# Kernel tuning notes

Hardware: AMD Instinct MI355X
Metric: run time of the kernel (lower is better)

The kernel has to match this reference:

```python
import jax, jax.numpy as jnp
import numpy as np

B, T, D = 4, 4096, 2048
E, C = 8, 512
O = 2048
I = D // E  # expert_in_features = 256


def setup_inputs() -> dict:
    key = jax.random.key(0)
    k1, k2, k3, k4, k5 = jax.random.split(key, 5)
    x = jax.random.normal(k1, (B, T, D), dtype=jnp.float32)
    combine_array = jax.random.uniform(k2, (B, T, E, C), dtype=jnp.float32)
    dispatch_mask = jax.random.uniform(k3, (B, T, E, C), dtype=jnp.float32)
    weight = jax.random.normal(k4, (E, O, I), dtype=jnp.float32) * (1.0 / np.sqrt(I))
    bias = jax.random.normal(k5, (O,), dtype=jnp.float32) * 0.01
    return {"x": x, "combine_array": combine_array, "dispatch_mask": dispatch_mask,
            "weight": weight, "bias": bias}


def reference(x, combine_array, dispatch_mask, weight, bias):
    b, t, d = x.shape
    e, o, i = weight.shape
    # dispatch: one-hot gather of tokens into expert capacity slots
    xr = x.reshape(b, t, e, i)                                   # [B,T,E,I]
    xd = jnp.einsum('btei,btec->beci', xr, dispatch_mask)        # [B,E,C,I]
    # bias homogenization trick: append 1 to features, bias column to weight
    x_homo = jnp.concatenate([xd, jnp.ones_like(xd[..., :1])], axis=-1)       # [B,E,C,I+1]
    b_col = jnp.broadcast_to(bias.reshape(1, o, 1), (e, o, 1))
    w_homo = jnp.concatenate([weight, b_col], axis=-1)                        # [E,O,I+1]
    # per-expert linear then combine scatter back to tokens
    y = jnp.einsum('beci,eoi->beco', x_homo, w_homo)             # [B,E,C,O]
    out = jnp.einsum('beco,btec->bto', y, combine_array)         # [B,T,O]
    return out
```

## Files before the change

kernel.cpp:

```cpp
#include <hip/hip_runtime.h>

typedef float f32x4 __attribute__((ext_vector_type(4)));
typedef short s16x8 __attribute__((ext_vector_type(8)));
typedef short s16x4 __attribute__((ext_vector_type(4)));
typedef unsigned u32x4 __attribute__((ext_vector_type(4)));
typedef unsigned u32x2 __attribute__((ext_vector_type(2)));

#define DEVI __device__ __forceinline__

static constexpr int B_ = 4, T_ = 4096, D_ = 2048, E_ = 8, C_ = 512, O_ = 2048, I_ = 256;
static constexpr size_t XDN = (size_t)B_ * E_ * I_ * C_;

DEVI short f2bf(float f) {
  unsigned u = __builtin_bit_cast(unsigned, f);
  u += 0x7FFFu + ((u >> 16) & 1u);
  return (short)(u >> 16);
}

DEVI unsigned cvtpk(float lo, float hi) {
  unsigned r;
  asm("v_cvt_pk_bf16_f32 %0, %1, %2" : "=v"(r) : "v"(lo), "v"(hi));
  return r;
}

DEVI void gll16(const short* gsrc, short* ldst) {
  __builtin_amdgcn_global_load_lds(
      (const __attribute__((address_space(1))) void*)gsrc,
      (__attribute__((address_space(3))) void*)ldst, 16, 0, 0);
}

__global__ __launch_bounds__(512, 2) void k_gemm1(const float* __restrict__ x,
                                                  const float* __restrict__ disp,
                                                  const float* __restrict__ w,
                                                  short* __restrict__ wT,
                                                  float* __restrict__ xdP) {
  __shared__ short lXT[128 * 64];
  __shared__ short lDT[256 * 64];
  const int tid = threadIdx.x;
  const int bid = blockIdx.x;

  if (bid >= 256) {
    const int pb = bid - 256;
#pragma unroll
    for (int u = 0; u < 2; u++) {
      const int idx = (pb * 512 + tid) * 2 + u;
      const int o = idx >> 9;
      const int dd = (idx & 511) << 2;
      const int e = dd >> 8, i = dd & 255;
      f32x4 v = *(const f32x4*)(w + (((size_t)e * O_ + o) * I_ + i));
      u32x2 p = {cvtpk(v[0], v[1]), cvtpk(v[2], v[3])};
      const int dsw = (dd & ~63) | (dd & 7) | ((((dd >> 3) & 7) ^ (o & 7)) << 3);
      *(u32x2*)(wT + (size_t)o * D_ + dsw) = p;
    }
    return;
  }

  const int xcd = bid & 7, slot = bid >> 3;
  const int grp = (slot >> 2) * 8 + xcd;
  const int jj = slot & 3;
  const int be = grp >> 1, kc = grp & 1;
  const int mt = jj >> 1, nt = jj & 1;
  const int b = be >> 3, e = be & 7;
  const int lane = tid & 63, wid = tid >> 6;
  const int wm = wid >> 2, wn = wid & 3;
  const int g = lane >> 4, lr = lane & 15;

  const size_t xbase = (size_t)b * T_ * D_ + (size_t)e * I_ + (size_t)mt * 128;
  const size_t dbase = (size_t)b * T_ * (E_ * C_) + (size_t)e * C_ + (size_t)nt * 256;

  const f32x4 z4 = {0.f, 0.f, 0.f, 0.f};
  f32x4 acc[4][4];
#pragma unroll
  for (int i = 0; i < 4; i++)
#pragma unroll
    for (int j = 0; j < 4; j++) acc[i][j] = z4;

  const int xt0 = (tid >> 4) * 2;
  const int xi8 = (tid & 15) * 8;
  const int dt0 = (tid >> 5) * 2;
  const int dc8 = (tid & 31) * 8;
  const int q7 = tid & 7;

  f32x4 xa0, xa1, xb0, xb1;
  f32x4 da[2][4];
  auto loadRegs = [&](int kt) {
    const float* sx = x + xbase + (size_t)(kt + xt0) * D_ + xi8;
    xa0 = *(const f32x4*)sx;
    xa1 = *(const f32x4*)(sx + 4);
    xb0 = *(const f32x4*)(sx + D_);
    xb1 = *(const f32x4*)(sx + D_ + 4);
#pragma unroll
    for (int tt = 0; tt < 2; tt++) {
      const float* sd = disp + dbase + (size_t)(kt + tt * 32 + dt0) * (E_ * C_) + dc8;
      da[tt][0] = *(const f32x4*)sd;
      da[tt][1] = *(const f32x4*)(sd + 4);
      da[tt][2] = *(const f32x4*)(sd + E_ * C_);
      da[tt][3] = *(const f32x4*)(sd + E_ * C_ + 4);
    }
  };
  auto writeLds = [&]() {
#pragma unroll
    for (int j = 0; j < 8; j++) {
      const int i = xi8 + j;
      const int ad = i * 64 + (xt0 ^ ((j ^ q7) << 3));
      float va = (j < 4) ? xa0[j] : xa1[j - 4];
      float vb = (j < 4) ? xb0[j] : xb1[j - 4];
      *(unsigned*)&lXT[ad] = cvtpk(va, vb);
    }
#pragma unroll
    for (int tt = 0; tt < 2; tt++)
#pragma unroll
      for (int j = 0; j < 8; j++) {
        const int c = dc8 + j;
        const int ad = c * 64 + ((tt * 32 + dt0) ^ ((j ^ q7) << 3));
        float ua = (j < 4) ? da[tt][0][j] : da[tt][1][j - 4];
        float ub = (j < 4) ? da[tt][2][j] : da[tt][3][j - 4];
        *(unsigned*)&lDT[ad] = cvtpk(ua, ub);
      }
  };

  const int k0 = kc * 2048, kend = k0 + 2048;
  loadRegs(k0);
  for (int kt = k0; kt < kend; kt += 64) {
    __syncthreads();
    writeLds();
    if (kt + 64 < kend) loadRegs(kt + 64);
    __syncthreads();
#pragma unroll
    for (int kk = 0; kk < 2; kk++) {
      const int tb = kk * 32 + g * 8;
      s16x8 af[4], bfr[4];
#pragma unroll
      for (int mi = 0; mi < 4; mi++) {
        const int r = wm * 64 + mi * 16 + lr;
        const int sws = (((r & 7) ^ ((r >> 3) & 7)) << 3);
        af[mi] = *(const s16x8*)&lXT[r * 64 + (tb ^ sws)];
      }
#pragma unroll
      for (int ni = 0; ni < 4; ni++) {
        const int r = wn * 64 + ni * 16 + lr;
        const int sws = (((r & 7) ^ ((r >> 3) & 7)) << 3);
        bfr[ni] = *(const s16x8*)&lDT[r * 64 + (tb ^ sws)];
      }
#pragma unroll
      for (int mi = 0; mi < 4; mi++)
#pragma unroll
        for (int ni = 0; ni < 4; ni++)
          acc[mi][ni] = __builtin_amdgcn_mfma_f32_16x16x32_bf16(af[mi], bfr[ni], acc[mi][ni], 0, 0, 0);
    }
  }

  float* op = xdP + (size_t)kc * XDN + (size_t)be * I_ * C_;
#pragma unroll
  for (int mi = 0; mi < 4; mi++)
#pragma unroll
    for (int ni = 0; ni < 4; ni++)
#pragma unroll
      for (int r = 0; r < 4; r++) {
        const int ig = mt * 128 + wm * 64 + mi * 16 + g * 4 + r;
        const int cg = nt * 256 + wn * 64 + ni * 16 + lr;
        op[(size_t)ig * C_ + cg] = acc[mi][ni][r];
      }
}

__global__ __launch_bounds__(256) void k_cvt(const float* __restrict__ xdP,
                                             short* __restrict__ xdT) {
  size_t idx = (size_t)blockIdx.x * 256 + threadIdx.x;
  f32x4 a = *(const f32x4*)(xdP + idx * 4);
  f32x4 b = *(const f32x4*)(xdP + XDN + idx * 4);
#pragma unroll
  for (int j = 0; j < 4; j++) a[j] += b[j];
  u32x2 p = {cvtpk(a[0], a[1]), cvtpk(a[2], a[3])};
  *(u32x2*)(xdT + idx * 4) = p;
}

__global__ __launch_bounds__(512, 2) void k_zgemm(const float* __restrict__ comb,
                                                  const short* __restrict__ xdT,
                                                  short* __restrict__ z,
                                                  float* __restrict__ Se) {
  __shared__ short lA[128 * 64];
  __shared__ short lB[256 * 64];
  const int tid = threadIdx.x;
  const int bid = blockIdx.x;
  const int be = bid >> 5, mt = bid & 31;
  const int b = be >> 3, e = be & 7;
  const int lane = tid & 63, wid = tid >> 6;
  const int wm = wid >> 2, wn = wid & 3;
  const int g = lane >> 4, lr = lane & 15;

  const size_t abase = (size_t)b * T_ * (E_ * C_) + (size_t)(mt * 128) * (E_ * C_) + (size_t)e * C_;
  const short* Bsrc = xdT + (size_t)be * I_ * C_;

  float rs[2] = {0.f, 0.f};
  const f32x4 z4 = {0.f, 0.f, 0.f, 0.f};
  f32x4 acc[4][4];
#pragma unroll
  for (int i = 0; i < 4; i++)
#pragma unroll
    for (int j = 0; j < 4; j++) acc[i][j] = z4;

  for (int ct = 0; ct < C_; ct += 64) {
    __syncthreads();
#pragma unroll
    for (int cc = 0; cc < 2; cc++) {
      const int q = tid + 512 * cc;
      const int row = q >> 3;
      const int k8 = (q & 7) << 3;
      const int sw = (row & 7) << 3;
      const float* sa = comb + abase + (size_t)row * (E_ * C_) + ct + k8;
      f32x4 a0 = *(const f32x4*)sa;
      f32x4 a1 = *(const f32x4*)(sa + 4);
      rs[cc] += a0[0] + a0[1] + a0[2] + a0[3] + a1[0] + a1[1] + a1[2] + a1[3];
      u32x4 pw = {cvtpk(a0[0], a0[1]), cvtpk(a0[2], a0[3]),
                  cvtpk(a1[0], a1[1]), cvtpk(a1[2], a1[3])};
      *(u32x4*)&lA[row * 64 + (k8 ^ sw)] = pw;
    }
#pragma unroll
    for (int cc = 0; cc < 4; cc++) {
      const int q = tid + 512 * cc;
      const int row = q >> 3;
      const int k8 = (q & 7) << 3;
      const int sw = (row & 7) << 3;
      s16x8 pb = *(const s16x8*)(Bsrc + (size_t)row * C_ + ct + k8);
      *(s16x8*)&lB[row * 64 + (k8 ^ sw)] = pb;
    }
    __syncthreads();
#pragma unroll
    for (int kk = 0; kk < 2; kk++) {
      const int kb = kk * 32 + g * 8;
      s16x8 af[4], bf[4];
#pragma unroll
      for (int mi = 0; mi < 4; mi++) {
        const int r = wm * 64 + mi * 16 + lr;
        af[mi] = *(const s16x8*)&lA[r * 64 + (kb ^ ((r & 7) << 3))];
      }
#pragma unroll
      for (int ni = 0; ni < 4; ni++) {
        const int r = wn * 64 + ni * 16 + lr;
        bf[ni] = *(const s16x8*)&lB[r * 64 + (kb ^ ((r & 7) << 3))];
      }
#pragma unroll
      for (int mi = 0; mi < 4; mi++)
#pragma unroll
        for (int ni = 0; ni < 4; ni++)
          acc[mi][ni] = __builtin_amdgcn_mfma_f32_16x16x32_bf16(af[mi], bf[ni], acc[mi][ni], 0, 0, 0);
    }
  }
#pragma unroll
  for (int cc = 0; cc < 2; cc++) {
    float v = rs[cc];
    v += __shfl_xor(v, 1);
    v += __shfl_xor(v, 2);
    v += __shfl_xor(v, 4);
    if ((tid & 7) == 0)
      Se[((size_t)b * E_ + e) * T_ + mt * 128 + (tid >> 3) + 64 * cc] = v;
  }
#pragma unroll
  for (int mi = 0; mi < 4; mi++)
#pragma unroll
    for (int ni = 0; ni < 4; ni++)
#pragma unroll
      for (int r = 0; r < 4; r++) {
        const int tg = mt * 128 + wm * 64 + mi * 16 + g * 4 + r;
        const int ig = wn * 64 + ni * 16 + lr;
        const int d = e * I_ + ig;
        const int dsw = (d & ~63) | (d & 7) | ((((d >> 3) & 7) ^ (tg & 7)) << 3);
        z[((size_t)b * T_ + tg) * D_ + dsw] = f2bf(acc[mi][ni][r]);
      }
}

__global__ __launch_bounds__(512, 2) void k_outgemm(const short* __restrict__ z,
                                                    const short* __restrict__ wT,
                                                    const float* __restrict__ bias,
                                                    const float* __restrict__ Se,
                                                    float* __restrict__ out) {
  __shared__ short lA[256 * 64];
  __shared__ short lB[256 * 64];
  const int tid = threadIdx.x;
  const int lane = tid & 63, wid = tid >> 6;
  const int wm = wid >> 2, wn = wid & 3;
  const int g = lane >> 4, lr = lane & 15;

  const int bid = blockIdx.x;
  const int swz = (bid & 7) * 64 + (bid >> 3);
  const int mt = swz >> 3, nt = swz & 7;
  const int row0 = mt * 256;
  const int col0 = nt * 256;

  const int srow = (wid << 4) + (lane >> 3);
  const int scol = (lane & 7) << 3;
  const short* Abase = z + (size_t)(row0 + srow) * D_ + scol;
  const short* Bbase = wT + (size_t)(col0 + srow) * D_ + scol;

  const f32x4 zero4 = {0.f, 0.f, 0.f, 0.f};
  f32x4 acc[8][4];
#pragma unroll
  for (int i = 0; i < 8; i++)
#pragma unroll
    for (int j = 0; j < 4; j++) acc[i][j] = zero4;

  s16x8 af[8], bf0[4], bf1[4];
  const int swr = (lr & 7) << 3;

  auto stage = [&](int dt) {
#pragma unroll
    for (int h = 0; h < 2; h++) {
      gll16(Abase + (size_t)(h * 128) * D_ + dt, &lA[(h * 128 + wid * 16) * 64]);
      gll16(Abase + (size_t)(h * 128 + 8) * D_ + dt, &lA[(h * 128 + wid * 16 + 8) * 64]);
      gll16(Bbase + (size_t)(h * 128) * D_ + dt, &lB[(h * 128 + wid * 16) * 64]);
      gll16(Bbase + (size_t)(h * 128 + 8) * D_ + dt, &lB[(h * 128 + wid * 16 + 8) * 64]);
    }
  };
  auto readA = [&](int mh) {
#pragma unroll
    for (int mi = 0; mi < 4; mi++) {
      const int r = mh * 128 + wm * 64 + mi * 16 + lr;
#pragma unroll
      for (int ks = 0; ks < 2; ks++)
        af[mi * 2 + ks] = *(const s16x8*)&lA[r * 64 + ((ks * 32 + g * 8) ^ swr)];
    }
  };
  auto readB = [&](int nh, s16x8* arr) {
#pragma unroll
    for (int ni = 0; ni < 2; ni++) {
      const int r = nh * 128 + wn * 32 + ni * 16 + lr;
#pragma unroll
      for (int ks = 0; ks < 2; ks++)
        arr[ni * 2 + ks] = *(const s16x8*)&lB[r * 64 + ((ks * 32 + g * 8) ^ swr)];
    }
  };
  auto mmaq = [&](int mh, int nh, const s16x8* bb) {
    __builtin_amdgcn_s_setprio(1);
#pragma unroll
    for (int mi = 0; mi < 4; mi++)
#pragma unroll
      for (int ni = 0; ni < 2; ni++)
#pragma unroll
        for (int ks = 0; ks < 2; ks++)
          acc[mh * 4 + mi][nh * 2 + ni] = __builtin_amdgcn_mfma_f32_16x16x32_bf16(
              af[mi * 2 + ks], bb[ni * 2 + ks], acc[mh * 4 + mi][nh * 2 + ni], 0, 0, 0);
    __builtin_amdgcn_s_setprio(0);
  };

  for (int t = 0; t < 32; ++t) {
    __syncthreads();
    stage(t * 64);
    __syncthreads();
    readA(0); readB(0, bf0);
    mmaq(0, 0, bf0);
    readB(1, bf1);
    mmaq(0, 1, bf1);
    readA(1);
    mmaq(1, 0, bf0);
    mmaq(1, 1, bf1);
  }

  __syncthreads();
  float* sS = (float*)lA;
  if (tid < 256) {
    const int bb = row0 >> 12, tt = (row0 & (T_ - 1)) + tid;
    float s = 0.f;
#pragma unroll
    for (int e = 0; e < E_; e++)
      s += Se[((size_t)(bb * E_ + e) << 12) + tt];
    sS[tid] = s;
  }
  __syncthreads();

  float bia[4];
#pragma unroll
  for (int nh = 0; nh < 2; nh++)
#pragma unroll
    for (int ni = 0; ni < 2; ni++)
      bia[nh * 2 + ni] = bias[col0 + nh * 128 + wn * 32 + ni * 16 + lr];
#pragma unroll
  for (int mh = 0; mh < 2; mh++)
#pragma unroll
    for (int mi = 0; mi < 4; mi++)
#pragma unroll
      for (int r = 0; r < 4; r++) {
        const int tg = row0 + mh * 128 + wm * 64 + mi * 16 + g * 4 + r;
        const float s = sS[tg - row0];
#pragma unroll
        for (int nh = 0; nh < 2; nh++)
#pragma unroll
          for (int ni = 0; ni < 2; ni++) {
            const int og = col0 + nh * 128 + wn * 32 + ni * 16 + lr;
            out[(size_t)tg * O_ + og] = acc[mh * 4 + mi][nh * 2 + ni][r] + bia[nh * 2 + ni] * s;
          }
      }
}

extern "C" void kernel_launch(void* const* d_in, const int* in_sizes, int n_in,
                              void* d_out, int out_size, void* d_ws, size_t ws_size,
                              hipStream_t stream) {
  const float* x    = (const float*)d_in[0];
  const float* comb = (const float*)d_in[1];
  const float* disp = (const float*)d_in[2];
  const float* w    = (const float*)d_in[3];
  const float* bias = (const float*)d_in[4];
  float* out = (float*)d_out;

  char* ws = (char*)d_ws;
  short* wT  = (short*)(ws);
  short* xdT = (short*)(ws + 8388608);
  short* z   = (short*)(ws + 16777216);
  float* xdP = (float*)(ws + 16777216);
  float* Se  = (float*)(ws + 83886080);

  k_gemm1<<<dim3(1280), dim3(512), 0, stream>>>(x, disp, w, wT, xdP);
  k_cvt<<<dim3(4096), dim3(256), 0, stream>>>(xdP, xdT);
  k_zgemm<<<dim3(1024), dim3(512), 0, stream>>>(comb, xdT, z, Se);
  k_outgemm<<<dim3(512), dim3(512), 0, stream>>>(z, wT, bias, Se, out);
}
```

Baseline: 368.3 us.

## Shrink output GEMM tile to 128x256 and double grid for occupancy

Reworks the output GEMM from 256x256 tiles with split half-tile MFMA scheduling to 128x256 tiles. Each wave computes a 64x64 sub-tile, the A LDS buffer is halved, and launch bounds ask for 4 blocks per CU. The grid doubles to 1024 blocks to improve occupancy and wave balance. In exchange, data reuse per tile drops, so more global and LDS traffic is needed per FLOP, and the hand-interleaved read/MFMA schedule is removed.

```diff
diff --git a/kernel.cpp b/kernel.cpp
--- a/kernel.cpp
+++ b/kernel.cpp
@@ -269,12 +269,12 @@
       }
 }
 
-__global__ __launch_bounds__(512, 2) void k_outgemm(const short* __restrict__ z,
+__global__ __launch_bounds__(512, 4) void k_outgemm(const short* __restrict__ z,
                                                     const short* __restrict__ wT,
                                                     const float* __restrict__ bias,
                                                     const float* __restrict__ Se,
                                                     float* __restrict__ out) {
-  __shared__ short lA[256 * 64];
+  __shared__ short lA[128 * 64];
   __shared__ short lB[256 * 64];
   const int tid = threadIdx.x;
   const int lane = tid & 63, wid = tid >> 6;
@@ -282,82 +282,57 @@
   const int g = lane >> 4, lr = lane & 15;
 
   const int bid = blockIdx.x;
-  const int swz = (bid & 7) * 64 + (bid >> 3);
+  const int swz = (bid & 7) * 128 + (bid >> 3);
   const int mt = swz >> 3, nt = swz & 7;
-  const int row0 = mt * 256;
+  const int row0 = mt * 128;
   const int col0 = nt * 256;
 
-  const int srow = (wid << 4) + (lane >> 3);
+  const int srow = lane >> 3;
   const int scol = (lane & 7) << 3;
-  const short* Abase = z + (size_t)(row0 + srow) * D_ + scol;
-  const short* Bbase = wT + (size_t)(col0 + srow) * D_ + scol;
+  const short* Abase = z + (size_t)(row0 + wid * 16 + srow) * D_ + scol;
+  const short* Bbase = wT + (size_t)(col0 + wid * 32 + srow) * D_ + scol;
 
   const f32x4 zero4 = {0.f, 0.f, 0.f, 0.f};
-  f32x4 acc[8][4];
-#pragma unroll
-  for (int i = 0; i < 8; i++)
+  f32x4 acc[4][4];
+#pragma unroll
+  for (int i = 0; i < 4; i++)
 #pragma unroll
     for (int j = 0; j < 4; j++) acc[i][j] = zero4;
 
-  s16x8 af[8], bf0[4], bf1[4];
-  const int swr = (lr & 7) << 3;
-
-  auto stage = [&](int dt) {
-#pragma unroll
-    for (int h = 0; h < 2; h++) {
-      gll16(Abase + (size_t)(h * 128) * D_ + dt, &lA[(h * 128 + wid * 16) * 64]);
-      gll16(Abase + (size_t)(h * 128 + 8) * D_ + dt, &lA[(h * 128 + wid * 16 + 8) * 64]);
-      gll16(Bbase + (size_t)(h * 128) * D_ + dt, &lB[(h * 128 + wid * 16) * 64]);
-      gll16(Bbase + (size_t)(h * 128 + 8) * D_ + dt, &lB[(h * 128 + wid * 16 + 8) * 64]);
-    }
-  };
-  auto readA = [&](int mh) {
-#pragma unroll
-    for (int mi = 0; mi < 4; mi++) {
-      const int r = mh * 128 + wm * 64 + mi * 16 + lr;
-#pragma unroll
-      for (int ks = 0; ks < 2; ks++)
-        af[mi * 2 + ks] = *(const s16x8*)&lA[r * 64 + ((ks * 32 + g * 8) ^ swr)];
-    }
-  };
-  auto readB = [&](int nh, s16x8* arr) {
-#pragma unroll
-    for (int ni = 0; ni < 2; ni++) {
-      const int r = nh * 128 + wn * 32 + ni * 16 + lr;
-#pragma unroll
-      for (int ks = 0; ks < 2; ks++)
-        arr[ni * 2 + ks] = *(const s16x8*)&lB[r * 64 + ((ks * 32 + g * 8) ^ swr)];
-    }
-  };
-  auto mmaq = [&](int mh, int nh, const s16x8* bb) {
-    __builtin_amdgcn_s_setprio(1);
-#pragma unroll
-    for (int mi = 0; mi < 4; mi++)
-#pragma unroll
-      for (int ni = 0; ni < 2; ni++)
-#pragma unroll
-        for (int ks = 0; ks < 2; ks++)
-          acc[mh * 4 + mi][nh * 2 + ni] = __builtin_amdgcn_mfma_f32_16x16x32_bf16(
-              af[mi * 2 + ks], bb[ni * 2 + ks], acc[mh * 4 + mi][nh * 2 + ni], 0, 0, 0);
-    __builtin_amdgcn_s_setprio(0);
-  };
-
   for (int t = 0; t < 32; ++t) {
-    __syncthreads();
-    stage(t * 64);
-    __syncthreads();
-    readA(0); readB(0, bf0);
-    mmaq(0, 0, bf0);
-    readB(1, bf1);
-    mmaq(0, 1, bf1);
-    readA(1);
-    mmaq(1, 0, bf0);
-    mmaq(1, 1, bf1);
+    const int dt = t * 64;
+    __syncthreads();
+    gll16(Abase + dt, &lA[(wid * 16 + srow) * 64]);
+    gll16(Abase + (size_t)8 * D_ + dt, &lA[(wid * 16 + 8 + srow) * 64]);
+#pragma unroll
+    for (int h = 0; h < 4; h++)
+      gll16(Bbase + (size_t)(h * 8) * D_ + dt, &lB[(wid * 32 + h * 8 + srow) * 64]);
+    __syncthreads();
+#pragma unroll
+    for (int kk = 0; kk < 2; kk++) {
+      const int kb = kk * 32 + g * 8;
+      s16x8 af[4], bf[4];
+#pragma unroll
+      for (int mi = 0; mi < 4; mi++) {
+        const int r = wm * 64 + mi * 16 + lr;
+        af[mi] = *(const s16x8*)&lA[r * 64 + (kb ^ ((r & 7) << 3))];
+      }
+#pragma unroll
+      for (int ni = 0; ni < 4; ni++) {
+        const int r = wn * 64 + ni * 16 + lr;
+        bf[ni] = *(const s16x8*)&lB[r * 64 + (kb ^ ((r & 7) << 3))];
+      }
+#pragma unroll
+      for (int mi = 0; mi < 4; mi++)
+#pragma unroll
+        for (int ni = 0; ni < 4; ni++)
+          acc[mi][ni] = __builtin_amdgcn_mfma_f32_16x16x32_bf16(af[mi], bf[ni], acc[mi][ni], 0, 0, 0);
+    }
   }
 
   __syncthreads();
   float* sS = (float*)lA;
-  if (tid < 256) {
+  if (tid < 128) {
     const int bb = row0 >> 12, tt = (row0 & (T_ - 1)) + tid;
     float s = 0.f;
 #pragma unroll
@@ -369,26 +344,20 @@
 
   float bia[4];
 #pragma unroll
-  for (int nh = 0; nh < 2; nh++)
-#pragma unroll
-    for (int ni = 0; ni < 2; ni++)
-      bia[nh * 2 + ni] = bias[col0 + nh * 128 + wn * 32 + ni * 16 + lr];
-#pragma unroll
-  for (int mh = 0; mh < 2; mh++)
-#pragma unroll
-    for (int mi = 0; mi < 4; mi++)
-#pragma unroll
-      for (int r = 0; r < 4; r++) {
-        const int tg = row0 + mh * 128 + wm * 64 + mi * 16 + g * 4 + r;
-        const float s = sS[tg - row0];
-#pragma unroll
-        for (int nh = 0; nh < 2; nh++)
-#pragma unroll
-          for (int ni = 0; ni < 2; ni++) {
-            const int og = col0 + nh * 128 + wn * 32 + ni * 16 + lr;
-            out[(size_t)tg * O_ + og] = acc[mh * 4 + mi][nh * 2 + ni][r] + bia[nh * 2 + ni] * s;
-          }
-      }
+  for (int ni = 0; ni < 4; ni++) bia[ni] = bias[col0 + wn * 64 + ni * 16 + lr];
+#pragma unroll
+  for (int mi = 0; mi < 4; mi++)
+#pragma unroll
+    for (int r = 0; r < 4; r++) {
+      const int rl = wm * 64 + mi * 16 + g * 4 + r;
+      const int tg = row0 + rl;
+      const float s = sS[rl];
+#pragma unroll
+      for (int ni = 0; ni < 4; ni++) {
+        const int og = col0 + wn * 64 + ni * 16 + lr;
+        out[(size_t)tg * O_ + og] = acc[mi][ni][r] + bia[ni] * s;
+      }
+    }
 }
 
 extern "C" void kernel_launch(void* const* d_in, const int* in_sizes, int n_in,
@@ -411,5 +380,5 @@
   k_gemm1<<<dim3(1280), dim3(512), 0, stream>>>(x, disp, w, wT, xdP);
   k_cvt<<<dim3(4096), dim3(256), 0, stream>>>(xdP, xdT);
   k_zgemm<<<dim3(1024), dim3(512), 0, stream>>>(comb, xdT, z, Se);
-  k_outgemm<<<dim3(512), dim3(512), 0, stream>>>(z, wT, bias, Se, out);
-}
+  k_outgemm<<<dim3(1024), dim3(512), 0, stream>>>(z, wT, bias, Se, out);
+}
```

Result: faster. 326.4 us (-11.4%).
